# Performance work log

Measured on AMD Instinct MI355X. Metric: run time of the kernel, lower is better.

Reference implementation:

```python
import jax, jax.numpy as jnp
import numpy as np
from jax import lax

BN_EPS = 1e-5

def _conv1d_same(x, w):
    # x: [N, 1, C], w: [1, 1, k] with k odd -> SAME padding along channel axis
    k = w.shape[-1]
    return lax.conv_general_dilated(x, w, window_strides=(1,),
                                    padding=[(k // 2, k // 2)],
                                    dimension_numbers=('NCH', 'OIH', 'NCH'))

def setup_inputs() -> dict:
    key = jax.random.key(0)
    ks = jax.random.split(key, 6)
    B, C, H, W = 4, 64, 64, 64
    kk = 3  # kernel size from in_dim=64: t=int(abs(log2(64)+1)/2)=3 (odd)
    x = jax.random.normal(ks[0], (B, C, H, W), dtype=jnp.float32)
    q_w = jax.random.normal(ks[1], (1, 1, kk), dtype=jnp.float32) * 0.5
    k_w = jax.random.normal(ks[2], (1, 1, kk), dtype=jnp.float32) * 0.5
    v_w = jax.random.normal(ks[3], (C, C), dtype=jnp.float32) * (1.0 / np.sqrt(C))
    v_b = jnp.zeros((C,), dtype=jnp.float32)
    gamma = jax.random.uniform(ks[4], (1,), dtype=jnp.float32, minval=0.5, maxval=1.5)
    bn_w = jnp.ones((C,), dtype=jnp.float32)
    bn_b = jnp.zeros((C,), dtype=jnp.float32)
    return {"x": x, "q_w": q_w, "k_w": k_w, "v_w": v_w, "v_b": v_b,
            "gamma": gamma, "bn_w": bn_w, "bn_b": bn_b}

def reference(x, q_w, k_w, v_w, v_b, gamma, bn_w, bn_b):
    B, C, H, W = x.shape
    N = H * W
    # conv1d Q/K projections over the channel axis, per spatial position
    xp = x.reshape(B, C, N).transpose(0, 2, 1).reshape(B * N, 1, C)
    q = _conv1d_same(xp, q_w).reshape(B, N, C)   # proj_query: [B, HW, C]
    k = _conv1d_same(xp, k_w).reshape(B, N, C)   # proj_key (pre-permute)
    energy = jnp.einsum('bnc,bmc->bnm', q, k)    # [B, HW, HW]
    attn = jax.nn.softmax(energy, axis=-1)
    # 1x1 value conv
    v = jnp.einsum('oc,bchw->bohw', v_w, x) + v_b[None, :, None, None]
    vv = v.reshape(B, C, N)
    # bmm(value, attention^T)
    out = jnp.einsum('bcm,bnm->bcn', vv, attn).reshape(B, C, H, W)
    y = gamma[0] * out
    # BatchNorm2d, training mode (batch statistics, biased variance)
    mean = jnp.mean(y, axis=(0, 2, 3), keepdims=True)
    var = jnp.var(y, axis=(0, 2, 3), keepdims=True)
    y = (y - mean) * lax.rsqrt(var + BN_EPS)
    y = y * bn_w[None, :, None, None] + bn_b[None, :, None, None]
    return y + x
```

## Files before the change

kernel.cpp:

```cpp
#include <hip/hip_runtime.h>
#include <stdint.h>

using f16 = _Float16;

typedef _Float16 f16x8 __attribute__((ext_vector_type(8)));
typedef _Float16 f16x4 __attribute__((ext_vector_type(4)));
typedef float f32x4 __attribute__((ext_vector_type(4)));

#define LOG2E 1.44269504088896340736f

__device__ __forceinline__ f16 f2h(float f) { return (f16)f; }

#if __has_builtin(__builtin_amdgcn_exp2f)
__device__ __forceinline__ float fexp2(float x) { return __builtin_amdgcn_exp2f(x); }
#else
__device__ __forceinline__ float fexp2(float x) { return exp2f(x); }
#endif

typedef __attribute__((address_space(1))) const uint32_t gu32;
typedef __attribute__((address_space(3))) uint32_t lu32;

__device__ __forceinline__ void dma16(const void* g, void* l) {
  __builtin_amdgcn_global_load_lds((gu32*)g, (lu32*)l, 16, 0, 0);
}

__device__ __forceinline__ f16x8 cvt8(const float* p) {
  const float4 a = *(const float4*)p;
  const float4 b = *(const float4*)(p + 4);
  f16x8 r;
  r[0] = (f16)a.x; r[1] = (f16)a.y; r[2] = (f16)a.z; r[3] = (f16)a.w;
  r[4] = (f16)b.x; r[5] = (f16)b.y; r[6] = (f16)b.z; r[7] = (f16)b.w;
  return r;
}


__global__ __launch_bounds__(256, 2) void pam_pre(
    const float* __restrict__ x, const float* __restrict__ qw,
    const float* __restrict__ kw, const float* __restrict__ vw,
    const float* __restrict__ vb,
    f16* __restrict__ qa, f16* __restrict__ ka2, f16* __restrict__ va3,
    float* __restrict__ gz)
{
  __shared__ alignas(16) f16 xt[16 * 72];
  const int tid = threadIdx.x;
  const int b = blockIdx.x >> 8;
  const int n0 = (blockIdx.x & 255) << 4;
  const int lane = tid & 63;
  const int wv = tid >> 6;
  const int quad = lane >> 4, l15 = lane & 15;

  if (blockIdx.x == 0 && tid < 128) gz[tid] = 0.f;

  {
    const int c = tid >> 2;
    const int j0 = (tid & 3) << 2;
    const float4 v0 = *(const float4*)(x + ((size_t)(b * 64 + c) << 12) + n0 + j0);
    xt[(j0 + 0) * 72 + c] = f2h(v0.x);
    xt[(j0 + 1) * 72 + c] = f2h(v0.y);
    xt[(j0 + 2) * 72 + c] = f2h(v0.z);
    xt[(j0 + 3) * 72 + c] = f2h(v0.w);
  }
  __syncthreads();

  if (tid < 128) {
    const float qw0 = qw[0], qw1 = qw[1], qw2 = qw[2];
    const float kw0 = kw[0], kw1 = kw[1], kw2 = kw[2];
    const int n = tid >> 3;
    const int c8 = tid & 7;
    const f16x8 v0 = *(const f16x8*)&xt[n * 72 + c8 * 8];
    const float lm = (c8 > 0) ? (float)xt[n * 72 + c8 * 8 - 1] : 0.f;
    const float rp = (c8 < 7) ? (float)xt[n * 72 + c8 * 8 + 8] : 0.f;
    f16x8 qv8, kv8;
#pragma unroll
    for (int j = 0; j < 8; ++j) {
      const float xm = (j == 0) ? lm : (float)v0[j - 1];
      const float x0 = (float)v0[j];
      const float xp = (j == 7) ? rp : (float)v0[j + 1];
      qv8[j] = f2h((qw0 * xm + qw1 * x0 + qw2 * xp) * LOG2E);
      kv8[j] = f2h(kw0 * xm + kw1 * x0 + kw2 * xp);
    }
    const int nn = n0 + n;
    *(f16x8*)(qa + ((size_t)((b << 12) + nn) << 6) + c8 * 8) = qv8;
    *(f16x8*)(ka2 + (((size_t)(b * 8 + c8)) << 15) + (nn << 3)) = kv8;
  }

  {
    const f16x8 a0 = *(const f16x8*)&xt[l15 * 72 + quad * 8];
    const f16x8 a1 = *(const f16x8*)&xt[l15 * 72 + quad * 8 + 32];
    const int co = wv * 16 + l15;
    const f16x8 b0 = cvt8(vw + co * 64 + quad * 8);
    const f16x8 b1 = cvt8(vw + co * 64 + quad * 8 + 32);
    f32x4 z = {0.f, 0.f, 0.f, 0.f};
    z = __builtin_amdgcn_mfma_f32_16x16x32_f16(a0, b0, z, 0, 0, 0);
    z = __builtin_amdgcn_mfma_f32_16x16x32_f16(a1, b1, z, 0, 0, 0);
    const float vbv = vb[co];
    f16x4 pv;
#pragma unroll
    for (int r = 0; r < 4; ++r) pv[r] = f2h(z[r] + vbv);
    const int nb = n0 + quad * 4;
    *(f16x4*)(va3 + (((size_t)(b * 512 + (nb >> 3))) << 9)
              + (co << 3) + (nb & 7)) = pv;
  }
}

__global__ __launch_bounds__(512, 4) void pam_attn(
    const f16* __restrict__ qa, const f16* __restrict__ ka2,
    const f16* __restrict__ va3, const float* __restrict__ gam,
    float* __restrict__ y0, float* __restrict__ gs1, float* __restrict__ gs2)
{
  __shared__ alignas(16) f16 kbuf[8][4096];
  __shared__ float ldsO[32 * 65];
  __shared__ float ldsM[4][32], ldsL[4][32], ldsMg[32], ldsInv[32];

  const int tid = threadIdx.x;
  const int wv = tid >> 6, lane = tid & 63;
  const int quad = lane >> 4, l15 = lane & 15;
  const int ks = wv & 3, qh = wv >> 2;
  const int b = blockIdx.x & 3;
  const int qb = blockIdx.x >> 2;
  const int qb0 = qb << 5;
  const int phase = qb & 31;

  for (int i = tid; i < 32 * 65; i += 512) ldsO[i] = 0.f;
  __syncthreads();

  const int bn = b << 12;
  f16x8 bq0, bq1;
  {
    const int q = qb0 + qh * 16 + l15;
    const f16* qp = qa + ((size_t)(bn + q) << 6) + quad * 8;
    bq0 = *(const f16x8*)qp;
    bq1 = *(const f16x8*)(qp + 32);
  }

  const int s31 = lane & 31;
  const int kmap = (((s31 & 15) >> 2) << 3) + (s31 & 3) + ((s31 >> 4) << 2);
  const f16* kgs = ka2 + (((size_t)(b * 8 + (lane >> 5))) << 15)
                 + ((ks * 32 + kmap) << 3);
  f16* const kwv = kbuf[wv];

  const f16* vgp = va3 + ((size_t)b << 18) + ((ks * 4 + quad) << 9) + (l15 << 3);

  f32x4 o[4] = {};
  float m = -1e30f, lp = 0.f;

  const int koff = ((quad >> 1) << 9) + ((quad & 1) << 8) + (l15 << 3);

  {
    const f16* src = kgs + ((size_t)phase << 10);
    dma16(src,          kwv);
    dma16(src + 65536,  kwv + 512);
    dma16(src + 131072, kwv + 1024);
    dma16(src + 196608, kwv + 1536);
  }

#pragma unroll 1
  for (int kt = 0; kt < 32; ++kt) {
    const int cur = kt & 1;
    const int gcur = (kt + phase) & 31;

    const f16* vt = vgp + ((size_t)gcur << 13);
    const f16x8 av0 = *(const f16x8*)(vt);
    const f16x8 av1 = *(const f16x8*)(vt + 128);
    const f16x8 av2 = *(const f16x8*)(vt + 256);
    const f16x8 av3 = *(const f16x8*)(vt + 384);
    __builtin_amdgcn_sched_barrier(0);

    asm volatile("s_waitcnt vmcnt(4)" ::: "memory");
    __builtin_amdgcn_sched_barrier(0);

    const f16* kc = kwv + (cur << 11);
    const f16x8 ak00 = *(const f16x8*)(kc + koff);
    const f16x8 ak01 = *(const f16x8*)(kc + koff + 1024);
    const f16x8 ak10 = *(const f16x8*)(kc + koff + 128);
    const f16x8 ak11 = *(const f16x8*)(kc + koff + 1152);

    f32x4 z0, z1;
    {
      f32x4 z = {0.f, 0.f, 0.f, 0.f};
      z = __builtin_amdgcn_mfma_f32_16x16x32_f16(ak00, bq0, z, 0, 0, 0);
      z0 = __builtin_amdgcn_mfma_f32_16x16x32_f16(ak01, bq1, z, 0, 0, 0);
    }
    {
      f32x4 z = {0.f, 0.f, 0.f, 0.f};
      z = __builtin_amdgcn_mfma_f32_16x16x32_f16(ak10, bq0, z, 0, 0, 0);
      z1 = __builtin_amdgcn_mfma_f32_16x16x32_f16(ak11, bq1, z, 0, 0, 0);
    }

    if (kt < 31) {
      const int tn = (kt + 1 + phase) & 31;
      const f16* src = kgs + ((size_t)tn << 10);
      f16* dst = kwv + ((cur ^ 1) << 11);
      dma16(src,          dst);
      dma16(src + 65536,  dst + 512);
      dma16(src + 131072, dst + 1024);
      dma16(src + 196608, dst + 1536);
    }

    float tmax = fmaxf(fmaxf(fmaxf(z0[0], z0[1]), fmaxf(z0[2], z0[3])),
                       fmaxf(fmaxf(z1[0], z1[1]), fmaxf(z1[2], z1[3])));
    tmax = fmaxf(tmax, __shfl_xor(tmax, 16, 64));
    tmax = fmaxf(tmax, __shfl_xor(tmax, 32, 64));
    const bool need = !__all(tmax <= m + 8.f);
    const float mn = need ? fmaxf(m, tmax) : m;

    const float p0 = fexp2(z0[0] - mn);
    const float p1 = fexp2(z0[1] - mn);
    const float p2 = fexp2(z0[2] - mn);
    const float p3 = fexp2(z0[3] - mn);
    const float p4 = fexp2(z1[0] - mn);
    const float p5 = fexp2(z1[1] - mn);
    const float p6 = fexp2(z1[2] - mn);
    const float p7 = fexp2(z1[3] - mn);
    const float ts = ((p0 + p1) + (p2 + p3)) + ((p4 + p5) + (p6 + p7));

    f16x8 pa;
    pa[0] = f2h(p0); pa[1] = f2h(p1); pa[2] = f2h(p2); pa[3] = f2h(p3);
    pa[4] = f2h(p4); pa[5] = f2h(p5); pa[6] = f2h(p6); pa[7] = f2h(p7);

    if (need) {
      const float al = fexp2(m - mn);
      lp = lp * al + ts;
      m = mn;
#pragma unroll
      for (int ct = 0; ct < 4; ++ct)
        for (int r = 0; r < 4; ++r) o[ct][r] *= al;
    } else {
      lp += ts;
    }

    o[0] = __builtin_amdgcn_mfma_f32_16x16x32_f16(av0, pa, o[0], 0, 0, 0);
    o[1] = __builtin_amdgcn_mfma_f32_16x16x32_f16(av1, pa, o[1], 0, 0, 0);
    o[2] = __builtin_amdgcn_mfma_f32_16x16x32_f16(av2, pa, o[2], 0, 0, 0);
    o[3] = __builtin_amdgcn_mfma_f32_16x16x32_f16(av3, pa, o[3], 0, 0, 0);
  }

  asm volatile("s_waitcnt vmcnt(0)" ::: "memory");

  {
    float v = lp;
    v += __shfl_xor(v, 16, 64);
    v += __shfl_xor(v, 32, 64);
    if (quad == 0) {
      ldsM[ks][qh * 16 + l15] = m;
      ldsL[ks][qh * 16 + l15] = v;
    }
  }
  __syncthreads();

  if (tid < 32) {
    const float M = fmaxf(fmaxf(ldsM[0][tid], ldsM[1][tid]),
                          fmaxf(ldsM[2][tid], ldsM[3][tid]));
    const float lt = ldsL[0][tid] * fexp2(ldsM[0][tid] - M) +
                     ldsL[1][tid] * fexp2(ldsM[1][tid] - M) +
                     ldsL[2][tid] * fexp2(ldsM[2][tid] - M) +
                     ldsL[3][tid] * fexp2(ldsM[3][tid] - M);
    ldsMg[tid] = M;
    ldsInv[tid] = 1.f / lt;
  }
  __syncthreads();

  {
    const int q = qh * 16 + l15;
    const float sc = fexp2(m - ldsMg[q]);
#pragma unroll
    for (int ct = 0; ct < 4; ++ct)
      for (int r = 0; r < 4; ++r)
        atomicAdd(&ldsO[q * 65 + ct * 16 + quad * 4 + r], o[ct][r] * sc);
  }
  __syncthreads();

  const float g = gam[0];
  {
    const int c = tid >> 3;
    const int q0 = (tid & 7) << 2;
    float4 v4;
    float* vp = &v4.x;
    float s1 = 0.f, s2 = 0.f;
    for (int r = 0; r < 4; ++r) {
      const float val = g * ldsO[(q0 + r) * 65 + c] * ldsInv[q0 + r];
      vp[r] = val; s1 += val; s2 += val * val;
    }
    *(float4*)(y0 + ((size_t)(b * 64 + c) << 12) + qb0 + q0) = v4;
    s1 += __shfl_xor(s1, 1, 64);
    s2 += __shfl_xor(s2, 1, 64);
    s1 += __shfl_xor(s1, 2, 64);
    s2 += __shfl_xor(s2, 2, 64);
    s1 += __shfl_xor(s1, 4, 64);
    s2 += __shfl_xor(s2, 4, 64);
    if ((tid & 7) == 0) {
      atomicAdd(&gs1[c], s1);
      atomicAdd(&gs2[c], s2);
    }
  }
}

__global__ __launch_bounds__(256, 2) void pam_apply(
    const float* __restrict__ y0, const float* __restrict__ x,
    const float* __restrict__ gs1, const float* __restrict__ gs2,
    const float* __restrict__ bnw, const float* __restrict__ bnb,
    float* __restrict__ out)
{
  const int i = (blockIdx.x * 256 + threadIdx.x) << 2;
  const int c = (i >> 12) & 63;
  const float inv_n = 1.f / 16384.f;
  const float mean = gs1[c] * inv_n;
  const float var = fmaxf(gs2[c] * inv_n - mean * mean, 0.f);
  const float sc = bnw[c] * rsqrtf(var + 1e-5f);
  const float sh = bnb[c] - mean * sc;
  const float4 y = *(const float4*)(y0 + i);
  const float4 xv = *(const float4*)(x + i);
  float4 r;
  r.x = y.x * sc + sh + xv.x;
  r.y = y.y * sc + sh + xv.y;
  r.z = y.z * sc + sh + xv.z;
  r.w = y.w * sc + sh + xv.w;
  *(float4*)(out + i) = r;
}

extern "C" void kernel_launch(void* const* d_in, const int* in_sizes, int n_in,
                              void* d_out, int out_size, void* d_ws, size_t ws_size,
                              hipStream_t stream)
{
  (void)in_sizes; (void)n_in; (void)out_size; (void)ws_size;
  const float* x   = (const float*)d_in[0];
  const float* qw  = (const float*)d_in[1];
  const float* kw  = (const float*)d_in[2];
  const float* vw  = (const float*)d_in[3];
  const float* vb  = (const float*)d_in[4];
  const float* gam = (const float*)d_in[5];
  const float* bnw = (const float*)d_in[6];
  const float* bnb = (const float*)d_in[7];

  char* ws = (char*)d_ws;
  f16*   qa  = (f16*)(ws);
  f16*   ka2 = (f16*)(ws + (2u << 20));
  f16*   va3 = (f16*)(ws + (4u << 20));
  float* y0  = (float*)(ws + (6u << 20));
  float* gs1 = (float*)(ws + (10u << 20));
  float* gs2 = (float*)(ws + (10u << 20) + 256);

  pam_pre  <<<1024, 256, 0, stream>>>(x, qw, kw, vw, vb, qa, ka2, va3, gs1);
  pam_attn <<<512, 512, 0, stream>>>(qa, ka2, va3, gam, y0, gs1, gs2);
  pam_apply<<<1024, 256, 0, stream>>>(y0, x, gs1, gs2, bnw, bnb, (float*)d_out);
}
```

Measured before the change: 150.4 us.

## Halve attention query tile to 16 and split keys across 8 waves

Each attention block now handles 16 queries instead of 32, and all 8 waves split the key range so each wave processes a 16-key slice per tile instead of 32. The grid doubles to 1024 blocks, per-block LDS shrinks, and the launch bound asks for 8 blocks per CU, aiming for more parallelism and occupancy. The PV product moves to the 16x16x16 MFMA with f16x4 operands, and the final merge combines 8 partial softmax states instead of 4. In exchange each wave does smaller MFMAs with more loop overhead per FLOP, and K/V tiles are re-read by twice as many blocks.

Result: slower. 185.1 us (+23.0%).

```diff
diff --git a/kernel.cpp b/kernel.cpp
--- a/kernel.cpp
+++ b/kernel.cpp
@@ -103,56 +103,51 @@
   }
 }
 
-__global__ __launch_bounds__(512, 4) void pam_attn(
+__global__ __launch_bounds__(512, 8) void pam_attn(
     const f16* __restrict__ qa, const f16* __restrict__ ka2,
     const f16* __restrict__ va3, const float* __restrict__ gam,
     float* __restrict__ y0, float* __restrict__ gs1, float* __restrict__ gs2)
 {
-  __shared__ alignas(16) f16 kbuf[8][4096];
-  __shared__ float ldsO[32 * 65];
-  __shared__ float ldsM[4][32], ldsL[4][32], ldsMg[32], ldsInv[32];
+  __shared__ alignas(16) f16 kbuf[8][2048];
+  __shared__ float ldsO[16 * 65];
+  __shared__ float ldsM[8][16], ldsL[8][16], ldsMg[16], ldsInv[16];
 
   const int tid = threadIdx.x;
   const int wv = tid >> 6, lane = tid & 63;
   const int quad = lane >> 4, l15 = lane & 15;
-  const int ks = wv & 3, qh = wv >> 2;
+  const int ks = wv;
   const int b = blockIdx.x & 3;
   const int qb = blockIdx.x >> 2;
-  const int qb0 = qb << 5;
+  const int qb0 = qb << 4;
   const int phase = qb & 31;
 
-  for (int i = tid; i < 32 * 65; i += 512) ldsO[i] = 0.f;
+  for (int i = tid; i < 16 * 65; i += 512) ldsO[i] = 0.f;
   __syncthreads();
 
   const int bn = b << 12;
   f16x8 bq0, bq1;
   {
-    const int q = qb0 + qh * 16 + l15;
+    const int q = qb0 + l15;
     const f16* qp = qa + ((size_t)(bn + q) << 6) + quad * 8;
     bq0 = *(const f16x8*)qp;
     bq1 = *(const f16x8*)(qp + 32);
   }
 
-  const int s31 = lane & 31;
-  const int kmap = (((s31 & 15) >> 2) << 3) + (s31 & 3) + ((s31 >> 4) << 2);
-  const f16* kgs = ka2 + (((size_t)(b * 8 + (lane >> 5))) << 15)
-                 + ((ks * 32 + kmap) << 3);
+  const f16* kgs0 = ka2 + (((size_t)(b * 8 + (lane >> 4))) << 15)
+                  + ((ks * 16 + (lane & 15)) << 3);
+  const f16* kgs1 = kgs0 + (4 << 15);
   f16* const kwv = kbuf[wv];
 
-  const f16* vgp = va3 + ((size_t)b << 18) + ((ks * 4 + quad) << 9) + (l15 << 3);
+  const f16* vgp = va3 + ((size_t)b << 18) + (((ks << 1) + (quad >> 1)) << 9)
+                 + (l15 << 3) + ((quad & 1) << 2);
 
   f32x4 o[4] = {};
   float m = -1e30f, lp = 0.f;
 
-  const int koff = ((quad >> 1) << 9) + ((quad & 1) << 8) + (l15 << 3);
-
-  {
-    const f16* src = kgs + ((size_t)phase << 10);
-    dma16(src,          kwv);
-    dma16(src + 65536,  kwv + 512);
-    dma16(src + 131072, kwv + 1024);
-    dma16(src + 196608, kwv + 1536);
-  }
+  const int koff = (quad << 7) + (l15 << 3);
+
+  dma16(kgs0 + ((size_t)phase << 10), kwv);
+  dma16(kgs1 + ((size_t)phase << 10), kwv + 512);
 
 #pragma unroll 1
   for (int kt = 0; kt < 32; ++kt) {
@@ -160,45 +155,34 @@
     const int gcur = (kt + phase) & 31;
 
     const f16* vt = vgp + ((size_t)gcur << 13);
-    const f16x8 av0 = *(const f16x8*)(vt);
-    const f16x8 av1 = *(const f16x8*)(vt + 128);
-    const f16x8 av2 = *(const f16x8*)(vt + 256);
-    const f16x8 av3 = *(const f16x8*)(vt + 384);
+    const f16x4 av0 = *(const f16x4*)(vt);
+    const f16x4 av1 = *(const f16x4*)(vt + 128);
+    const f16x4 av2 = *(const f16x4*)(vt + 256);
+    const f16x4 av3 = *(const f16x4*)(vt + 384);
     __builtin_amdgcn_sched_barrier(0);
 
     asm volatile("s_waitcnt vmcnt(4)" ::: "memory");
     __builtin_amdgcn_sched_barrier(0);
 
-    const f16* kc = kwv + (cur << 11);
-    const f16x8 ak00 = *(const f16x8*)(kc + koff);
-    const f16x8 ak01 = *(const f16x8*)(kc + koff + 1024);
-    const f16x8 ak10 = *(const f16x8*)(kc + koff + 128);
-    const f16x8 ak11 = *(const f16x8*)(kc + koff + 1152);
-
-    f32x4 z0, z1;
+    const f16* kc = kwv + (cur << 10);
+    const f16x8 ak0 = *(const f16x8*)(kc + koff);
+    const f16x8 ak1 = *(const f16x8*)(kc + 512 + koff);
+
+    f32x4 z0;
     {
       f32x4 z = {0.f, 0.f, 0.f, 0.f};
-      z = __builtin_amdgcn_mfma_f32_16x16x32_f16(ak00, bq0, z, 0, 0, 0);
-      z0 = __builtin_amdgcn_mfma_f32_16x16x32_f16(ak01, bq1, z, 0, 0, 0);
-    }
-    {
-      f32x4 z = {0.f, 0.f, 0.f, 0.f};
-      z = __builtin_amdgcn_mfma_f32_16x16x32_f16(ak10, bq0, z, 0, 0, 0);
-      z1 = __builtin_amdgcn_mfma_f32_16x16x32_f16(ak11, bq1, z, 0, 0, 0);
+      z = __builtin_amdgcn_mfma_f32_16x16x32_f16(ak0, bq0, z, 0, 0, 0);
+      z0 = __builtin_amdgcn_mfma_f32_16x16x32_f16(ak1, bq1, z, 0, 0, 0);
     }
 
     if (kt < 31) {
-      const int tn = (kt + 1 + phase) & 31;
-      const f16* src = kgs + ((size_t)tn << 10);
-      f16* dst = kwv + ((cur ^ 1) << 11);
-      dma16(src,          dst);
-      dma16(src + 65536,  dst + 512);
-      dma16(src + 131072, dst + 1024);
-      dma16(src + 196608, dst + 1536);
-    }
-
-    float tmax = fmaxf(fmaxf(fmaxf(z0[0], z0[1]), fmaxf(z0[2], z0[3])),
-                       fmaxf(fmaxf(z1[0], z1[1]), fmaxf(z1[2], z1[3])));
+      const size_t off = (size_t)((kt + 1 + phase) & 31) << 10;
+      f16* dst = kwv + ((cur ^ 1) << 10);
+      dma16(kgs0 + off, dst);
+      dma16(kgs1 + off, dst + 512);
+    }
+
+    float tmax = fmaxf(fmaxf(z0[0], z0[1]), fmaxf(z0[2], z0[3]));
     tmax = fmaxf(tmax, __shfl_xor(tmax, 16, 64));
     tmax = fmaxf(tmax, __shfl_xor(tmax, 32, 64));
     const bool need = !__all(tmax <= m + 8.f);
@@ -208,15 +192,10 @@
     const float p1 = fexp2(z0[1] - mn);
     const float p2 = fexp2(z0[2] - mn);
     const float p3 = fexp2(z0[3] - mn);
-    const float p4 = fexp2(z1[0] - mn);
-    const float p5 = fexp2(z1[1] - mn);
-    const float p6 = fexp2(z1[2] - mn);
-    const float p7 = fexp2(z1[3] - mn);
-    const float ts = ((p0 + p1) + (p2 + p3)) + ((p4 + p5) + (p6 + p7));
-
-    f16x8 pa;
+    const float ts = (p0 + p1) + (p2 + p3);
+
+    f16x4 pa;
     pa[0] = f2h(p0); pa[1] = f2h(p1); pa[2] = f2h(p2); pa[3] = f2h(p3);
-    pa[4] = f2h(p4); pa[5] = f2h(p5); pa[6] = f2h(p6); pa[7] = f2h(p7);
 
     if (need) {
       const float al = fexp2(m - mn);
@@ -229,10 +208,10 @@
       lp += ts;
     }
 
-    o[0] = __builtin_amdgcn_mfma_f32_16x16x32_f16(av0, pa, o[0], 0, 0, 0);
-    o[1] = __builtin_amdgcn_mfma_f32_16x16x32_f16(av1, pa, o[1], 0, 0, 0);
-    o[2] = __builtin_amdgcn_mfma_f32_16x16x32_f16(av2, pa, o[2], 0, 0, 0);
-    o[3] = __builtin_amdgcn_mfma_f32_16x16x32_f16(av3, pa, o[3], 0, 0, 0);
+    o[0] = __builtin_amdgcn_mfma_f32_16x16x16f16(av0, pa, o[0], 0, 0, 0);
+    o[1] = __builtin_amdgcn_mfma_f32_16x16x16f16(av1, pa, o[1], 0, 0, 0);
+    o[2] = __builtin_amdgcn_mfma_f32_16x16x16f16(av2, pa, o[2], 0, 0, 0);
+    o[3] = __builtin_amdgcn_mfma_f32_16x16x16f16(av3, pa, o[3], 0, 0, 0);
   }
 
   asm volatile("s_waitcnt vmcnt(0)" ::: "memory");
@@ -242,26 +221,26 @@
     v += __shfl_xor(v, 16, 64);
     v += __shfl_xor(v, 32, 64);
     if (quad == 0) {
-      ldsM[ks][qh * 16 + l15] = m;
-      ldsL[ks][qh * 16 + l15] = v;
-    }
-  }
-  __syncthreads();
-
-  if (tid < 32) {
-    const float M = fmaxf(fmaxf(ldsM[0][tid], ldsM[1][tid]),
-                          fmaxf(ldsM[2][tid], ldsM[3][tid]));
-    const float lt = ldsL[0][tid] * fexp2(ldsM[0][tid] - M) +
-                     ldsL[1][tid] * fexp2(ldsM[1][tid] - M) +
-                     ldsL[2][tid] * fexp2(ldsM[2][tid] - M) +
-                     ldsL[3][tid] * fexp2(ldsM[3][tid] - M);
+      ldsM[ks][l15] = m;
+      ldsL[ks][l15] = v;
+    }
+  }
+  __syncthreads();
+
+  if (tid < 16) {
+    float M = ldsM[0][tid];
+#pragma unroll
+    for (int k = 1; k < 8; ++k) M = fmaxf(M, ldsM[k][tid]);
+    float lt = 0.f;
+#pragma unroll
+    for (int k = 0; k < 8; ++k) lt += ldsL[k][tid] * fexp2(ldsM[k][tid] - M);
     ldsMg[tid] = M;
     ldsInv[tid] = 1.f / lt;
   }
   __syncthreads();
 
   {
-    const int q = qh * 16 + l15;
+    const int q = l15;
     const float sc = fexp2(m - ldsMg[q]);
 #pragma unroll
     for (int ct = 0; ct < 4; ++ct)
@@ -273,15 +252,16 @@
   const float g = gam[0];
   {
     const int c = tid >> 3;
-    const int q0 = (tid & 7) << 2;
-    float4 v4;
-    float* vp = &v4.x;
+    const int q0 = (tid & 7) << 1;
+    float2 v2;
     float s1 = 0.f, s2 = 0.f;
-    for (int r = 0; r < 4; ++r) {
-      const float val = g * ldsO[(q0 + r) * 65 + c] * ldsInv[q0 + r];
-      vp[r] = val; s1 += val; s2 += val * val;
-    }
-    *(float4*)(y0 + ((size_t)(b * 64 + c) << 12) + qb0 + q0) = v4;
+    {
+      const float v0 = g * ldsO[(q0 + 0) * 65 + c] * ldsInv[q0 + 0];
+      const float v1 = g * ldsO[(q0 + 1) * 65 + c] * ldsInv[q0 + 1];
+      v2.x = v0; v2.y = v1;
+      s1 = v0 + v1; s2 = v0 * v0 + v1 * v1;
+    }
+    *(float2*)(y0 + ((size_t)(b * 64 + c) << 12) + qb0 + q0) = v2;
     s1 += __shfl_xor(s1, 1, 64);
     s2 += __shfl_xor(s2, 1, 64);
     s1 += __shfl_xor(s1, 2, 64);
@@ -341,6 +321,6 @@
   float* gs2 = (float*)(ws + (10u << 20) + 256);
 
   pam_pre  <<<1024, 256, 0, stream>>>(x, qw, kw, vw, vb, qa, ka2, va3, gs1);
-  pam_attn <<<512, 512, 0, stream>>>(qa, ka2, va3, gam, y0, gs1, gs2);
+  pam_attn <<<1024, 512, 0, stream>>>(qa, ka2, va3, gam, y0, gs1, gs2);
   pam_apply<<<1024, 256, 0, stream>>>(y0, x, gs1, gs2, bnw, bnb, (float*)d_out);
 }
```
